# Optimization experiments

Measured on AMD Instinct MI355X. Metric: run time of the kernel, lower is better.

The kernel has to match this reference:

```python
import math
import jax, jax.numpy as jnp
import numpy as np

B, R, L_, K_, U_ = 64, 32, 64, 16, 4
DIMS = [2 * K_ * U_, 256, 256, K_]  # [input_dim] + hidden_dim + [output_dim]
BN_EPS = 1e-5


def _uniform_param(key, out_dim, in_dim):
    ini = math.sqrt(3.0 / out_dim / in_dim)
    return jax.random.uniform(key, (out_dim, in_dim), jnp.float32, -ini, ini)


def setup_inputs() -> dict:
    key = jax.random.key(0)
    ks = jax.random.split(key, 16)
    inp = {
        "Hhat_real": jax.random.normal(ks[0], (B, R, L_, K_, U_), jnp.float32),
        "Hhat_imag": jax.random.normal(ks[1], (B, R, L_, K_, U_), jnp.float32),
        "Vhat": jax.random.normal(ks[2], (B, R, L_, K_, U_), jnp.float32),
    }
    kidx = 3
    for i in range(len(DIMS) - 1):
        inp[f"P1_{i}"] = _uniform_param(ks[kidx], DIMS[i + 1], DIMS[i]); kidx += 1
        inp[f"P2_{i}"] = _uniform_param(ks[kidx], DIMS[i + 1], DIMS[i]); kidx += 1
        if i != len(DIMS) - 2:  # BN only on non-final layers
            inp[f"bn_w{i}"] = jnp.ones((DIMS[i + 1],), jnp.float32)
            inp[f"bn_b{i}"] = jnp.zeros((DIMS[i + 1],), jnp.float32)
    inp["nbrOfRealizations"] = R
    inp["L"] = L_
    inp["K"] = K_
    inp["U"] = U_
    return inp


def _layer(A, P1, P2, bn_w, bn_b, relu):
    # A: [N, C_in, L]
    A1 = jnp.einsum('oc,ncl->nol', P1, A)                       # [N, C_out, L]
    A2 = jnp.einsum('oc,nc->no', P2, A.mean(-1))[:, :, None]    # [N, C_out, 1]
    A = A1 + 0.1 * A2
    if relu:
        A = jax.nn.relu(A)
    if bn_w is not None:
        # BatchNorm1d (training mode): normalize over (N, L) per channel
        mu = A.mean(axis=(0, 2), keepdims=True)
        var = A.var(axis=(0, 2), keepdims=True)
        A = (A - mu) * jax.lax.rsqrt(var + BN_EPS) * bn_w[None, :, None] + bn_b[None, :, None]
    return A


def reference(Hhat_real, Hhat_imag, Vhat,
              P1_0, P2_0, bn_w0, bn_b0,
              P1_1, P2_1, bn_w1, bn_b1,
              P1_2, P2_2,
              nbrOfRealizations, L, K, U):
    Bsz = Hhat_real.shape[0]
    N = Bsz * nbrOfRealizations

    def prep(X):
        # view(N,1,L,K,U).transpose(2,3).transpose(3,4) -> [N,1,K,U,L]
        return jnp.transpose(X.reshape(N, 1, L, K, U), (0, 1, 3, 4, 2))

    A = jnp.concatenate([prep(Hhat_real), prep(Hhat_imag)], axis=1).reshape(N, 2 * K * U, L)
    A = _layer(A, P1_0, P2_0, bn_w0, bn_b0, relu=True)
    A = _layer(A, P1_1, P2_1, bn_w1, bn_b1, relu=True)
    A = _layer(A, P1_2, P2_2, None, None, relu=False)

    Phat_u1 = jnp.transpose(A.reshape(Bsz, nbrOfRealizations, K, L), (0, 1, 3, 2))  # [B,R,L,K]
    nrm = jnp.linalg.norm(Phat_u1, axis=2, keepdims=True)                            # [B,R,1,K]
    Phat_u = Phat_u1 / nrm * jnp.float32(math.sqrt(L))
    Fhat_u = Vhat.reshape(Bsz, nbrOfRealizations, L, K, U) * Phat_u[..., None]
    return Fhat_u
```

## Files before the change

kernel.cpp:

```cpp
#include <hip/hip_runtime.h>

typedef unsigned short ushort_t;
typedef unsigned int uint_t;

typedef short bf16x8 __attribute__((ext_vector_type(8)));
typedef float f32x4 __attribute__((ext_vector_type(4)));
#define MFMA16(a, b, c) __builtin_amdgcn_mfma_f32_16x16x32_bf16(a, b, c, 0, 0, 0)

__device__ __forceinline__ float bf2f(uint_t u) { return __uint_as_float(u << 16); }
__device__ __forceinline__ ushort_t f2bf(float f) {
  uint_t x = __float_as_uint(f);
  return (ushort_t)((x + 0x7fffu + ((x >> 16) & 1u)) >> 16);
}
__device__ __forceinline__ uint_t cvtpk(float lo, float hi) {
  uint_t r;
  asm("v_cvt_pk_bf16_f32 %0, %1, %2" : "=v"(r) : "v"(lo), "v"(hi));
  return r;
}
__device__ __forceinline__ void gload_lds16(const void* g, void* l) {
  __builtin_amdgcn_global_load_lds(
      (const __attribute__((address_space(1))) unsigned int*)g,
      (__attribute__((address_space(3))) unsigned int*)l, 16, 0, 0);
}

#define NBATCH 2048

__global__ __launch_bounds__(256) void pre0_kernel(
    const float* __restrict__ Hr, const float* __restrict__ Hi,
    const float* __restrict__ P2_0, const float* __restrict__ P1_0,
    ushort_t* __restrict__ W0bf, float* __restrict__ V20)
{
  __shared__ float r[4][128];
  __shared__ float hm[128];
  const int t = threadIdx.x, n = blockIdx.x;
  if (n < 128) {
    int i = n * 256 + t;
    W0bf[i] = f2bf(P1_0[i]);
  }
  const int q = t >> 6;
  const int c = (2 * t) & 127;
  const int cc = c & 63;
  const float* src = ((c < 64) ? Hr : Hi) + (size_t)n * 4096 + cc;
  float s0 = 0.f, s1 = 0.f;
  #pragma unroll
  for (int i = 0; i < 16; i++) {
    int l = 4 * i + q;
    float2 x = *(const float2*)(src + l * 64);
    s0 += x.x; s1 += x.y;
  }
  r[q][c] = s0; r[q][c + 1] = s1;
  __syncthreads();
  if (t < 128) hm[t] = (r[0][t] + r[1][t] + r[2][t] + r[3][t]) * (1.0f / 64.0f);
  __syncthreads();
  const float4* pw = (const float4*)(P2_0 + t * 128);
  float s = 0.f;
  #pragma unroll 8
  for (int c4 = 0; c4 < 32; c4++) {
    float4 p = pw[c4];
    s = fmaf(p.x, hm[4 * c4 + 0], s);
    s = fmaf(p.y, hm[4 * c4 + 1], s);
    s = fmaf(p.z, hm[4 * c4 + 2], s);
    s = fmaf(p.w, hm[4 * c4 + 3], s);
  }
  V20[n * 256 + t] = 0.1f * s;
}

__global__ __launch_bounds__(256) void layer0_mfma_kernel(
    const float* __restrict__ Hr, const float* __restrict__ Hi,
    const ushort_t* __restrict__ W0bf, const float* __restrict__ V20,
    ushort_t* __restrict__ Z, float* __restrict__ partA, float* __restrict__ partB)
{
  __shared__ __align__(16) ushort_t lds[64 * 264];
  float* ldsf = (float*)lds;
  const int t = threadIdx.x, n = blockIdx.x;
  const int lane = t & 63, w = t >> 6, r16 = lane & 15, g4 = lane >> 4;

  #pragma unroll
  for (int i = 0; i < 8; i++) {
    int G = (w * 8 + i) * 64 + lane;
    int row = G >> 5;
    int gc = G & 31;
    int gsrc = gc ^ (row & 7);
    int fi = gsrc * 4;
    const float* src = ((fi < 64) ? Hr : Hi) + (size_t)n * 4096 + row * 64 + (fi & 63);
    gload_lds16(src, &ldsf[(w * 8 + i) * 256]);
  }

  float4 v2r[4];
  #pragma unroll
  for (int m = 0; m < 4; m++)
    v2r[m] = *(const float4*)(V20 + n * 256 + w * 64 + m * 16 + g4 * 4);

  f32x4 acc[4][4];
  #pragma unroll
  for (int i = 0; i < 4; i++)
    #pragma unroll
    for (int j = 0; j < 4; j++) acc[i][j] = (f32x4){0.f, 0.f, 0.f, 0.f};

  __syncthreads();

  const int sw = r16 & 7;
  #pragma unroll
  for (int kk = 0; kk < 4; kk++) {
    bf16x8 aF[4], bF[4];
    #pragma unroll
    for (int m = 0; m < 4; m++)
      aF[m] = *(const bf16x8*)(W0bf + (w * 64 + m * 16 + r16) * 128 + kk * 32 + g4 * 8);
    #pragma unroll
    for (int nt = 0; nt < 4; nt++) {
      const int row = nt * 16 + r16;
      const float* base = ldsf + row * 128;
      const int g0 = kk * 8 + g4 * 2;
      float4 xa = *(const float4*)(base + ((g0 ^ sw) * 4));
      float4 xb = *(const float4*)(base + (((g0 + 1) ^ sw) * 4));
      uint4 u = make_uint4(cvtpk(xa.x, xa.y), cvtpk(xa.z, xa.w),
                           cvtpk(xb.x, xb.y), cvtpk(xb.z, xb.w));
      bF[nt] = *(const bf16x8*)&u;
    }
    #pragma unroll
    for (int m = 0; m < 4; m++)
      #pragma unroll
      for (int nt = 0; nt < 4; nt++)
        acc[m][nt] = MFMA16(aF[m], bF[nt], acc[m][nt]);
  }

  #pragma unroll
  for (int m = 0; m < 4; m++) {
    float s[4] = {0.f, 0.f, 0.f, 0.f}, q[4] = {0.f, 0.f, 0.f, 0.f};
    #pragma unroll
    for (int nt = 0; nt < 4; nt++)
      #pragma unroll
      for (int r = 0; r < 4; r++) {
        float v = fmaxf(acc[m][nt][r] + v2r[m][r], 0.f);
        s[r] += v; q[r] = fmaf(v, v, q[r]);
      }
    #pragma unroll
    for (int b = 1; b < 16; b <<= 1)
      #pragma unroll
      for (int r = 0; r < 4; r++) {
        s[r] += __shfl_xor(s[r], b);
        q[r] += __shfl_xor(q[r], b);
      }
    const int ob = w * 64 + m * 16 + g4 * 4;
    #pragma unroll
    for (int r = 0; r < 4; r++)
      if (r16 == r) {
        partA[n * 256 + ob + r] = s[r];
        partB[n * 256 + ob + r] = q[r];
      }
  }

  __syncthreads();
  #pragma unroll
  for (int m = 0; m < 4; m++) {
    const int ob = w * 64 + m * 16 + g4 * 4;
    #pragma unroll
    for (int nt = 0; nt < 4; nt++) {
      const int l = nt * 16 + r16;
      uint_t p0 = cvtpk(fmaxf(acc[m][nt][0] + v2r[m].x, 0.f),
                        fmaxf(acc[m][nt][1] + v2r[m].y, 0.f));
      uint_t p1 = cvtpk(fmaxf(acc[m][nt][2] + v2r[m].z, 0.f),
                        fmaxf(acc[m][nt][3] + v2r[m].w, 0.f));
      *(uint2*)(&lds[l * 264 + ob]) = make_uint2(p0, p1);
    }
  }
  __syncthreads();
  #pragma unroll
  for (int i = 0; i < 8; i++) {
    int el = i * 2048 + t * 8;
    int l = el >> 8, o0 = el & 255;
    *(uint4*)(&Z[(size_t)n * 16384 + el]) = *(const uint4*)(&lds[l * 264 + o0]);
  }
}

__global__ __launch_bounds__(256) void statsfin_kernel(
    const float* __restrict__ partA, const float* __restrict__ partB,
    const float* __restrict__ bnw, const float* __restrict__ bnb,
    float* __restrict__ stats)
{
  __shared__ float s1s[256], s2s[256];
  const int c = blockIdx.x, t = threadIdx.x;
  float s1 = 0.f, s2 = 0.f;
  #pragma unroll
  for (int j = 0; j < 8; j++) {
    int n = t * 8 + j;
    s1 += partA[n * 256 + c];
    s2 += partB[n * 256 + c];
  }
  s1s[t] = s1; s2s[t] = s2;
  __syncthreads();
  for (int s = 128; s > 0; s >>= 1) {
    if (t < s) { s1s[t] += s1s[t + s]; s2s[t] += s2s[t + s]; }
    __syncthreads();
  }
  if (t == 0) {
    const float inv = 1.0f / 131072.0f;
    float mu = s1s[0] * inv;
    float var = fmaxf(s2s[0] * inv - mu * mu, 0.f);
    float rstd = rsqrtf(var + 1e-5f);
    float sc = rstd * bnw[c];
    stats[2 * c]     = sc;
    stats[2 * c + 1] = bnb[c] - mu * sc;
  }
}

__global__ __launch_bounds__(256) void prep_kernel(
    const float* __restrict__ P1f, const float* __restrict__ P2f,
    const float* __restrict__ stats, ushort_t* __restrict__ Wbf,
    float* __restrict__ P2s, float* __restrict__ biasT)
{
  const int o = blockIdx.x, t = threadIdx.x;
  float sc = stats[2 * t], sh = stats[2 * t + 1];
  float w = P1f[o * 256 + t];
  Wbf[o * 256 + t] = f2bf(w * sc);
  float p = P2f[o * 256 + t];
  P2s[o * 256 + t] = p * sc;
  __shared__ float s1[256], s2[256];
  s1[t] = w * sh;
  s2[t] = p * sh;
  __syncthreads();
  for (int s = 128; s > 0; s >>= 1) {
    if (t < s) { s1[t] += s1[t + s]; s2[t] += s2[t + s]; }
    __syncthreads();
  }
  if (t == 0) biasT[o] = s1[0] + 0.1f * s2[0];
}

__global__ __launch_bounds__(256) void v2n_kernel(
    const float* __restrict__ partA, const float* __restrict__ P2s,
    const float* __restrict__ biasT, float* __restrict__ V2)
{
  __shared__ float zm[4][256];
  const int t = threadIdx.x, n0 = blockIdx.x * 4;
  #pragma unroll
  for (int j = 0; j < 4; j++) zm[j][t] = partA[(n0 + j) * 256 + t] * (1.0f / 64.0f);
  __syncthreads();
  float s[4] = {0.f, 0.f, 0.f, 0.f};
  const float4* pw = (const float4*)(P2s + t * 256);
  #pragma unroll 4
  for (int c4 = 0; c4 < 64; c4++) {
    float4 p = pw[c4];
    #pragma unroll
    for (int j = 0; j < 4; j++) {
      s[j] = fmaf(p.x, zm[j][4 * c4 + 0], s[j]);
      s[j] = fmaf(p.y, zm[j][4 * c4 + 1], s[j]);
      s[j] = fmaf(p.z, zm[j][4 * c4 + 2], s[j]);
      s[j] = fmaf(p.w, zm[j][4 * c4 + 3], s[j]);
    }
  }
  float b = biasT[t];
  #pragma unroll
  for (int j = 0; j < 4; j++) V2[(n0 + j) * 256 + t] = 0.1f * s[j] + b;
}

__global__ __launch_bounds__(256) void layer1_mfma_kernel(
    ushort_t* Z, const ushort_t* __restrict__ W1bf, const float* __restrict__ V21,
    float* __restrict__ partA, float* __restrict__ partB)
{
  __shared__ __align__(16) ushort_t lds[64 * 264];
  const int t = threadIdx.x, n = blockIdx.x;
  const int lane = t & 63, w = t >> 6, r16 = lane & 15, g4 = lane >> 4;
  const size_t zbase = (size_t)n * 16384;

  #pragma unroll
  for (int i = 0; i < 8; i++) {
    int G = (w * 8 + i) * 64 + lane;
    int row = G >> 5;
    int gc = G & 31;
    int gsrc = gc ^ (row & 7);
    gload_lds16(Z + zbase + row * 256 + gsrc * 8, &lds[(w * 8 + i) * 512]);
  }

  float4 v2r[4];
  #pragma unroll
  for (int m = 0; m < 4; m++)
    v2r[m] = *(const float4*)(V21 + n * 256 + w * 64 + m * 16 + g4 * 4);

  f32x4 acc[4][4];
  #pragma unroll
  for (int i = 0; i < 4; i++)
    #pragma unroll
    for (int j = 0; j < 4; j++) acc[i][j] = (f32x4){0.f, 0.f, 0.f, 0.f};

  bf16x8 aF[2][4];
  #pragma unroll
  for (int m = 0; m < 4; m++)
    aF[0][m] = *(const bf16x8*)(W1bf + (w * 64 + m * 16 + r16) * 256 + g4 * 8);

  __syncthreads();

  const int sw = r16 & 7;
  #pragma unroll
  for (int kk = 0; kk < 8; kk++) {
    const int cur = kk & 1, nxt = cur ^ 1;
    if (kk < 7) {
      #pragma unroll
      for (int m = 0; m < 4; m++)
        aF[nxt][m] = *(const bf16x8*)(W1bf + (w * 64 + m * 16 + r16) * 256 + (kk + 1) * 32 + g4 * 8);
    }
    bf16x8 bF[4];
    #pragma unroll
    for (int nt = 0; nt < 4; nt++) {
      const int row = nt * 16 + r16;
      bF[nt] = *(const bf16x8*)(&lds[row * 256 + (((kk * 4 + g4) ^ sw) * 8)]);
    }
    #pragma unroll
    for (int m = 0; m < 4; m++)
      #pragma unroll
      for (int nt = 0; nt < 4; nt++)
        acc[m][nt] = MFMA16(aF[cur][m], bF[nt], acc[m][nt]);
  }

  #pragma unroll
  for (int m = 0; m < 4; m++) {
    float s[4] = {0.f, 0.f, 0.f, 0.f}, q[4] = {0.f, 0.f, 0.f, 0.f};
    #pragma unroll
    for (int nt = 0; nt < 4; nt++)
      #pragma unroll
      for (int r = 0; r < 4; r++) {
        float v = fmaxf(acc[m][nt][r] + v2r[m][r], 0.f);
        s[r] += v; q[r] = fmaf(v, v, q[r]);
      }
    #pragma unroll
    for (int b = 1; b < 16; b <<= 1)
      #pragma unroll
      for (int r = 0; r < 4; r++) {
        s[r] += __shfl_xor(s[r], b);
        q[r] += __shfl_xor(q[r], b);
      }
    const int ob = w * 64 + m * 16 + g4 * 4;
    #pragma unroll
    for (int r = 0; r < 4; r++)
      if (r16 == r) {
        partA[n * 256 + ob + r] = s[r];
        partB[n * 256 + ob + r] = q[r];
      }
  }

  __syncthreads();
  #pragma unroll
  for (int m = 0; m < 4; m++) {
    const int ob = w * 64 + m * 16 + g4 * 4;
    #pragma unroll
    for (int nt = 0; nt < 4; nt++) {
      const int l = nt * 16 + r16;
      uint_t p0 = cvtpk(fmaxf(acc[m][nt][0] + v2r[m].x, 0.f),
                        fmaxf(acc[m][nt][1] + v2r[m].y, 0.f));
      uint_t p1 = cvtpk(fmaxf(acc[m][nt][2] + v2r[m].z, 0.f),
                        fmaxf(acc[m][nt][3] + v2r[m].w, 0.f));
      *(uint2*)(&lds[l * 264 + ob]) = make_uint2(p0, p1);
    }
  }
  __syncthreads();
  #pragma unroll
  for (int i = 0; i < 8; i++) {
    int el = i * 2048 + t * 8;
    int l = el >> 8, o0 = el & 255;
    *(uint4*)(&Z[zbase + el]) = *(const uint4*)(&lds[l * 264 + o0]);
  }
}

__global__ __launch_bounds__(256) void layer2final_kernel(
    const ushort_t* __restrict__ Z, const ushort_t* __restrict__ W2bf,
    const float* __restrict__ partA, const float* __restrict__ P2s2,
    const float* __restrict__ biasT2, const float* __restrict__ Vh,
    float* __restrict__ out)
{
  __shared__ float zm[256];
  __shared__ float red[16][17];
  __shared__ float v2s[16];
  __shared__ float zf[16][65];
  __shared__ float invn[16];
  const int t = threadIdx.x, n = blockIdx.x;
  const int lane = t & 63, w = t >> 6, r16 = lane & 15, g4 = lane >> 4;
  const size_t zbase = (size_t)n * 16384;

  zm[t] = partA[n * 256 + t] * (1.0f / 64.0f);

  f32x4 acc = (f32x4){0.f, 0.f, 0.f, 0.f};
  #pragma unroll 2
  for (int kk = 0; kk < 8; kk++) {
    bf16x8 aF = *(const bf16x8*)(W2bf + r16 * 256 + kk * 32 + g4 * 8);
    bf16x8 bF = *(const bf16x8*)(Z + zbase + (w * 16 + r16) * 256 + kk * 32 + g4 * 8);
    acc = MFMA16(aF, bF, acc);
  }
  __syncthreads();
  {
    const int oi = t & 15, ch = t >> 4;
    const float4* pw = (const float4*)(P2s2 + oi * 256 + ch * 16);
    float s = 0.f;
    #pragma unroll
    for (int c4 = 0; c4 < 4; c4++) {
      float4 p = pw[c4];
      int cb = ch * 16 + c4 * 4;
      s = fmaf(p.x, zm[cb + 0], s);
      s = fmaf(p.y, zm[cb + 1], s);
      s = fmaf(p.z, zm[cb + 2], s);
      s = fmaf(p.w, zm[cb + 3], s);
    }
    red[ch][oi] = s;
  }
  __syncthreads();
  if (t < 16) {
    float a = 0.f;
    #pragma unroll
    for (int c = 0; c < 16; c++) a += red[c][t];
    v2s[t] = 0.1f * a + biasT2[t];
  }
  __syncthreads();
  #pragma unroll
  for (int r = 0; r < 4; r++) {
    int o = g4 * 4 + r;
    zf[o][w * 16 + r16] = acc[r] + v2s[o];
  }
  __syncthreads();
  if (t < 16) {
    float s = 0.f;
    #pragma unroll
    for (int l = 0; l < 64; l++) s = fmaf(zf[t][l], zf[t][l], s);
    invn[t] = (s > 0.f) ? (8.0f * rsqrtf(s)) : 0.f;
  }
  __syncthreads();
  const size_t base = (size_t)n * 4096;
  #pragma unroll
  for (int g = 0; g < 4; g++) {
    int e = t * 16 + g * 4;
    int l = e >> 6;
    int k = (e >> 2) & 15;
    float val = zf[k][l] * invn[k];
    float4 vv = *(const float4*)(Vh + base + e);
    *(float4*)(out + base + e) =
        make_float4(vv.x * val, vv.y * val, vv.z * val, vv.w * val);
  }
}

extern "C" void kernel_launch(void* const* d_in, const int* in_sizes, int n_in,
                              void* d_out, int out_size, void* d_ws, size_t ws_size,
                              hipStream_t stream) {
  const float* Hr   = (const float*)d_in[0];
  const float* Hi   = (const float*)d_in[1];
  const float* Vh   = (const float*)d_in[2];
  const float* P1_0 = (const float*)d_in[3];
  const float* P2_0 = (const float*)d_in[4];
  const float* bnw0 = (const float*)d_in[5];
  const float* bnb0 = (const float*)d_in[6];
  const float* P1_1 = (const float*)d_in[7];
  const float* P2_1 = (const float*)d_in[8];
  const float* bnw1 = (const float*)d_in[9];
  const float* bnb1 = (const float*)d_in[10];
  const float* P1_2 = (const float*)d_in[11];
  const float* P2_2 = (const float*)d_in[12];

  char* ws = (char*)d_ws;
  float*    stats0 = (float*)   (ws);
  float*    stats1 = (float*)   (ws + 2048);
  float*    biasT  = (float*)   (ws + 4096);
  float*    biasT2 = (float*)   (ws + 5120);
  ushort_t* W0bf   = (ushort_t*)(ws + 8192);
  ushort_t* W1bf   = (ushort_t*)(ws + 73728);
  ushort_t* W2bf   = (ushort_t*)(ws + 204800);
  float*    P2s1   = (float*)   (ws + 212992);
  float*    P2s2   = (float*)   (ws + 475136);
  float*    partA  = (float*)   (ws + 491520);
  float*    partB  = (float*)   (ws + 2588672);
  float*    V20    = (float*)   (ws + 4685824);
  float*    V21    = (float*)   (ws + 6782976);
  ushort_t* Z      = (ushort_t*)(ws + 9437184);

  pre0_kernel<<<NBATCH, 256, 0, stream>>>(Hr, Hi, P2_0, P1_0, W0bf, V20);
  layer0_mfma_kernel<<<NBATCH, 256, 0, stream>>>(Hr, Hi, W0bf, V20, Z, partA, partB);
  statsfin_kernel<<<256, 256, 0, stream>>>(partA, partB, bnw0, bnb0, stats0);
  prep_kernel<<<256, 256, 0, stream>>>(P1_1, P2_1, stats0, W1bf, P2s1, biasT);
  v2n_kernel<<<512, 256, 0, stream>>>(partA, P2s1, biasT, V21);
  layer1_mfma_kernel<<<NBATCH, 256, 0, stream>>>(Z, W1bf, V21, partA, partB);
  statsfin_kernel<<<256, 256, 0, stream>>>(partA, partB, bnw1, bnb1, stats1);
  prep_kernel<<<16, 256, 0, stream>>>(P1_2, P2_2, stats1, W2bf, P2s2, biasT2);
  layer2final_kernel<<<NBATCH, 256, 0, stream>>>(Z, W2bf, partA, P2s2, biasT2, Vh, (float*)d_out);
}
```

Baseline: 206.7 us.

## Process two samples per block with double-buffered LDS prefetch in layers 0 and 1

Layer 0 and layer 1 MFMA kernels now handle two consecutive samples per block. Both samples get their own LDS buffer, and the second sample's global-to-LDS load is issued while the first sample is computed and written out. The grid is halved to match. The aim is to hide global load latency inside the block, at the cost of doubling LDS per block, which lowers the number of resident blocks per CU and halves the block count.

```diff
diff --git a/kernel.cpp b/kernel.cpp
--- a/kernel.cpp
+++ b/kernel.cpp
@@ -70,106 +70,116 @@
     const ushort_t* __restrict__ W0bf, const float* __restrict__ V20,
     ushort_t* __restrict__ Z, float* __restrict__ partA, float* __restrict__ partB)
 {
-  __shared__ __align__(16) ushort_t lds[64 * 264];
-  float* ldsf = (float*)lds;
-  const int t = threadIdx.x, n = blockIdx.x;
+  __shared__ __align__(16) ushort_t lds[2][64 * 264];
+  const int t = threadIdx.x, nb = blockIdx.x;
   const int lane = t & 63, w = t >> 6, r16 = lane & 15, g4 = lane >> 4;
-
-  #pragma unroll
-  for (int i = 0; i < 8; i++) {
-    int G = (w * 8 + i) * 64 + lane;
-    int row = G >> 5;
-    int gc = G & 31;
-    int gsrc = gc ^ (row & 7);
-    int fi = gsrc * 4;
-    const float* src = ((fi < 64) ? Hr : Hi) + (size_t)n * 4096 + row * 64 + (fi & 63);
-    gload_lds16(src, &ldsf[(w * 8 + i) * 256]);
-  }
-
-  float4 v2r[4];
-  #pragma unroll
-  for (int m = 0; m < 4; m++)
-    v2r[m] = *(const float4*)(V20 + n * 256 + w * 64 + m * 16 + g4 * 4);
-
-  f32x4 acc[4][4];
-  #pragma unroll
-  for (int i = 0; i < 4; i++)
-    #pragma unroll
-    for (int j = 0; j < 4; j++) acc[i][j] = (f32x4){0.f, 0.f, 0.f, 0.f};
-
-  __syncthreads();
-
   const int sw = r16 & 7;
-  #pragma unroll
-  for (int kk = 0; kk < 4; kk++) {
-    bf16x8 aF[4], bF[4];
+
+  auto stageH = [&](float* bufF, int n) {
+    #pragma unroll
+    for (int i = 0; i < 8; i++) {
+      int G = (w * 8 + i) * 64 + lane;
+      int row = G >> 5;
+      int gc = G & 31;
+      int gsrc = gc ^ (row & 7);
+      int fi = gsrc * 4;
+      const float* src = ((fi < 64) ? Hr : Hi) + (size_t)n * 4096 + row * 64 + (fi & 63);
+      gload_lds16(src, bufF + (w * 8 + i) * 256);
+    }
+  };
+
+  stageH((float*)&lds[0][0], 2 * nb);
+  __syncthreads();
+  stageH((float*)&lds[1][0], 2 * nb + 1);
+
+  #pragma unroll
+  for (int half = 0; half < 2; half++) {
+    const int n = 2 * nb + half;
+    ushort_t* buf = &lds[half][0];
+    float* bufF = (float*)buf;
+
+    float4 v2r[4];
     #pragma unroll
     for (int m = 0; m < 4; m++)
-      aF[m] = *(const bf16x8*)(W0bf + (w * 64 + m * 16 + r16) * 128 + kk * 32 + g4 * 8);
-    #pragma unroll
-    for (int nt = 0; nt < 4; nt++) {
-      const int row = nt * 16 + r16;
-      const float* base = ldsf + row * 128;
-      const int g0 = kk * 8 + g4 * 2;
-      float4 xa = *(const float4*)(base + ((g0 ^ sw) * 4));
-      float4 xb = *(const float4*)(base + (((g0 + 1) ^ sw) * 4));
-      uint4 u = make_uint4(cvtpk(xa.x, xa.y), cvtpk(xa.z, xa.w),
-                           cvtpk(xb.x, xb.y), cvtpk(xb.z, xb.w));
-      bF[nt] = *(const bf16x8*)&u;
-    }
-    #pragma unroll
-    for (int m = 0; m < 4; m++)
+      v2r[m] = *(const float4*)(V20 + n * 256 + w * 64 + m * 16 + g4 * 4);
+
+    f32x4 acc[4][4];
+    #pragma unroll
+    for (int i = 0; i < 4; i++)
+      #pragma unroll
+      for (int j = 0; j < 4; j++) acc[i][j] = (f32x4){0.f, 0.f, 0.f, 0.f};
+
+    #pragma unroll
+    for (int kk = 0; kk < 4; kk++) {
+      bf16x8 aF[4], bF[4];
+      #pragma unroll
+      for (int m = 0; m < 4; m++)
+        aF[m] = *(const bf16x8*)(W0bf + (w * 64 + m * 16 + r16) * 128 + kk * 32 + g4 * 8);
+      #pragma unroll
+      for (int nt = 0; nt < 4; nt++) {
+        const int row = nt * 16 + r16;
+        const float* base = bufF + row * 128;
+        const int g0 = kk * 8 + g4 * 2;
+        float4 xa = *(const float4*)(base + ((g0 ^ sw) * 4));
+        float4 xb = *(const float4*)(base + (((g0 + 1) ^ sw) * 4));
+        uint4 u = make_uint4(cvtpk(xa.x, xa.y), cvtpk(xa.z, xa.w),
+                             cvtpk(xb.x, xb.y), cvtpk(xb.z, xb.w));
+        bF[nt] = *(const bf16x8*)&u;
+      }
+      #pragma unroll
+      for (int m = 0; m < 4; m++)
+        #pragma unroll
+        for (int nt = 0; nt < 4; nt++)
+          acc[m][nt] = MFMA16(aF[m], bF[nt], acc[m][nt]);
+    }
+
+    #pragma unroll
+    for (int m = 0; m < 4; m++) {
+      float s[4] = {0.f, 0.f, 0.f, 0.f}, q[4] = {0.f, 0.f, 0.f, 0.f};
       #pragma unroll
       for (int nt = 0; nt < 4; nt++)
-        acc[m][nt] = MFMA16(aF[m], bF[nt], acc[m][nt]);
-  }
-
-  #pragma unroll
-  for (int m = 0; m < 4; m++) {
-    float s[4] = {0.f, 0.f, 0.f, 0.f}, q[4] = {0.f, 0.f, 0.f, 0.f};
-    #pragma unroll
-    for (int nt = 0; nt < 4; nt++)
-      #pragma unroll
-      for (int r = 0; r < 4; r++) {
-        float v = fmaxf(acc[m][nt][r] + v2r[m][r], 0.f);
-        s[r] += v; q[r] = fmaf(v, v, q[r]);
+        #pragma unroll
+        for (int r = 0; r < 4; r++) {
+          float v = fmaxf(acc[m][nt][r] + v2r[m][r], 0.f);
+          s[r] += v; q[r] = fmaf(v, v, q[r]);
+        }
+      #pragma unroll
+      for (int b = 1; b < 16; b <<= 1)
+        #pragma unroll
+        for (int r = 0; r < 4; r++) {
+          s[r] += __shfl_xor(s[r], b);
+          q[r] += __shfl_xor(q[r], b);
+        }
+      const int ob = w * 64 + m * 16 + g4 * 4;
+      #pragma unroll
+      for (int r = 0; r < 4; r++)
+        if (r16 == r) {
+          partA[n * 256 + ob + r] = s[r];
+          partB[n * 256 + ob + r] = q[r];
+        }
+    }
+
+    __syncthreads();
+    #pragma unroll
+    for (int m = 0; m < 4; m++) {
+      const int ob = w * 64 + m * 16 + g4 * 4;
+      #pragma unroll
+      for (int nt = 0; nt < 4; nt++) {
+        const int l = nt * 16 + r16;
+        uint_t p0 = cvtpk(fmaxf(acc[m][nt][0] + v2r[m].x, 0.f),
+                          fmaxf(acc[m][nt][1] + v2r[m].y, 0.f));
+        uint_t p1 = cvtpk(fmaxf(acc[m][nt][2] + v2r[m].z, 0.f),
+                          fmaxf(acc[m][nt][3] + v2r[m].w, 0.f));
+        *(uint2*)(&buf[l * 264 + ob]) = make_uint2(p0, p1);
       }
-    #pragma unroll
-    for (int b = 1; b < 16; b <<= 1)
-      #pragma unroll
-      for (int r = 0; r < 4; r++) {
-        s[r] += __shfl_xor(s[r], b);
-        q[r] += __shfl_xor(q[r], b);
-      }
-    const int ob = w * 64 + m * 16 + g4 * 4;
-    #pragma unroll
-    for (int r = 0; r < 4; r++)
-      if (r16 == r) {
-        partA[n * 256 + ob + r] = s[r];
-        partB[n * 256 + ob + r] = q[r];
-      }
-  }
-
-  __syncthreads();
-  #pragma unroll
-  for (int m = 0; m < 4; m++) {
-    const int ob = w * 64 + m * 16 + g4 * 4;
-    #pragma unroll
-    for (int nt = 0; nt < 4; nt++) {
-      const int l = nt * 16 + r16;
-      uint_t p0 = cvtpk(fmaxf(acc[m][nt][0] + v2r[m].x, 0.f),
-                        fmaxf(acc[m][nt][1] + v2r[m].y, 0.f));
-      uint_t p1 = cvtpk(fmaxf(acc[m][nt][2] + v2r[m].z, 0.f),
-                        fmaxf(acc[m][nt][3] + v2r[m].w, 0.f));
-      *(uint2*)(&lds[l * 264 + ob]) = make_uint2(p0, p1);
-    }
-  }
-  __syncthreads();
-  #pragma unroll
-  for (int i = 0; i < 8; i++) {
-    int el = i * 2048 + t * 8;
-    int l = el >> 8, o0 = el & 255;
-    *(uint4*)(&Z[(size_t)n * 16384 + el]) = *(const uint4*)(&lds[l * 264 + o0]);
+    }
+    __syncthreads();
+    #pragma unroll
+    for (int i = 0; i < 8; i++) {
+      int el = i * 2048 + t * 8;
+      int l = el >> 8, o0 = el & 255;
+      *(uint4*)(&Z[(size_t)n * 16384 + el]) = *(const uint4*)(&buf[l * 264 + o0]);
+    }
   }
 }
 
@@ -257,106 +267,117 @@
     ushort_t* Z, const ushort_t* __restrict__ W1bf, const float* __restrict__ V21,
     float* __restrict__ partA, float* __restrict__ partB)
 {
-  __shared__ __align__(16) ushort_t lds[64 * 264];
-  const int t = threadIdx.x, n = blockIdx.x;
+  __shared__ __align__(16) ushort_t lds[2][64 * 264];
+  const int t = threadIdx.x, nb = blockIdx.x;
   const int lane = t & 63, w = t >> 6, r16 = lane & 15, g4 = lane >> 4;
-  const size_t zbase = (size_t)n * 16384;
-
-  #pragma unroll
-  for (int i = 0; i < 8; i++) {
-    int G = (w * 8 + i) * 64 + lane;
-    int row = G >> 5;
-    int gc = G & 31;
-    int gsrc = gc ^ (row & 7);
-    gload_lds16(Z + zbase + row * 256 + gsrc * 8, &lds[(w * 8 + i) * 512]);
-  }
-
-  float4 v2r[4];
-  #pragma unroll
-  for (int m = 0; m < 4; m++)
-    v2r[m] = *(const float4*)(V21 + n * 256 + w * 64 + m * 16 + g4 * 4);
-
-  f32x4 acc[4][4];
-  #pragma unroll
-  for (int i = 0; i < 4; i++)
-    #pragma unroll
-    for (int j = 0; j < 4; j++) acc[i][j] = (f32x4){0.f, 0.f, 0.f, 0.f};
-
-  bf16x8 aF[2][4];
-  #pragma unroll
-  for (int m = 0; m < 4; m++)
-    aF[0][m] = *(const bf16x8*)(W1bf + (w * 64 + m * 16 + r16) * 256 + g4 * 8);
-
-  __syncthreads();
-
   const int sw = r16 & 7;
-  #pragma unroll
-  for (int kk = 0; kk < 8; kk++) {
-    const int cur = kk & 1, nxt = cur ^ 1;
-    if (kk < 7) {
+
+  auto stageZ = [&](ushort_t* buf, int n) {
+    const size_t zb = (size_t)n * 16384;
+    #pragma unroll
+    for (int i = 0; i < 8; i++) {
+      int G = (w * 8 + i) * 64 + lane;
+      int row = G >> 5;
+      int gc = G & 31;
+      int gsrc = gc ^ (row & 7);
+      gload_lds16(Z + zb + row * 256 + gsrc * 8, buf + (w * 8 + i) * 512);
+    }
+  };
+
+  stageZ(&lds[0][0], 2 * nb);
+  __syncthreads();
+  stageZ(&lds[1][0], 2 * nb + 1);
+
+  #pragma unroll
+  for (int half = 0; half < 2; half++) {
+    const int n = 2 * nb + half;
+    ushort_t* buf = &lds[half][0];
+    const size_t zbase = (size_t)n * 16384;
+
+    float4 v2r[4];
+    #pragma unroll
+    for (int m = 0; m < 4; m++)
+      v2r[m] = *(const float4*)(V21 + n * 256 + w * 64 + m * 16 + g4 * 4);
+
+    f32x4 acc[4][4];
+    #pragma unroll
+    for (int i = 0; i < 4; i++)
+      #pragma unroll
+      for (int j = 0; j < 4; j++) acc[i][j] = (f32x4){0.f, 0.f, 0.f, 0.f};
+
+    bf16x8 aF[2][4];
+    #pragma unroll
+    for (int m = 0; m < 4; m++)
+      aF[0][m] = *(const bf16x8*)(W1bf + (w * 64 + m * 16 + r16) * 256 + g4 * 8);
+
+    #pragma unroll
+    for (int kk = 0; kk < 8; kk++) {
+      const int cur = kk & 1, nxt = cur ^ 1;
+      if (kk < 7) {
+        #pragma unroll
+        for (int m = 0; m < 4; m++)
+          aF[nxt][m] = *(const bf16x8*)(W1bf + (w * 64 + m * 16 + r16) * 256 + (kk + 1) * 32 + g4 * 8);
+      }
+      bf16x8 bF[4];
+      #pragma unroll
+      for (int nt = 0; nt < 4; nt++) {
+        const int row = nt * 16 + r16;
+        bF[nt] = *(const bf16x8*)(&buf[row * 256 + (((kk * 4 + g4) ^ sw) * 8)]);
+      }
       #pragma unroll
       for (int m = 0; m < 4; m++)
-        aF[nxt][m] = *(const bf16x8*)(W1bf + (w * 64 + m * 16 + r16) * 256 + (kk + 1) * 32 + g4 * 8);
-    }
-    bf16x8 bF[4];
-    #pragma unroll
-    for (int nt = 0; nt < 4; nt++) {
-      const int row = nt * 16 + r16;
-      bF[nt] = *(const bf16x8*)(&lds[row * 256 + (((kk * 4 + g4) ^ sw) * 8)]);
-    }
-    #pragma unroll
-    for (int m = 0; m < 4; m++)
+        #pragma unroll
+        for (int nt = 0; nt < 4; nt++)
+          acc[m][nt] = MFMA16(aF[cur][m], bF[nt], acc[m][nt]);
+    }
+
+    #pragma unroll
+    for (int m = 0; m < 4; m++) {
+      float s[4] = {0.f, 0.f, 0.f, 0.f}, q[4] = {0.f, 0.f, 0.f, 0.f};
       #pragma unroll
       for (int nt = 0; nt < 4; nt++)
-        acc[m][nt] = MFMA16(aF[cur][m], bF[nt], acc[m][nt]);
-  }
-
-  #pragma unroll
-  for (int m = 0; m < 4; m++) {
-    float s[4] = {0.f, 0.f, 0.f, 0.f}, q[4] = {0.f, 0.f, 0.f, 0.f};
-    #pragma unroll
-    for (int nt = 0; nt < 4; nt++)
-      #pragma unroll
-      for (int r = 0; r < 4; r++) {
-        float v = fmaxf(acc[m][nt][r] + v2r[m][r], 0.f);
-        s[r] += v; q[r] = fmaf(v, v, q[r]);
+        #pragma unroll
+        for (int r = 0; r < 4; r++) {
+          float v = fmaxf(acc[m][nt][r] + v2r[m][r], 0.f);
+          s[r] += v; q[r] = fmaf(v, v, q[r]);
+        }
+      #pragma unroll
+      for (int b = 1; b < 16; b <<= 1)
+        #pragma unroll
+        for (int r = 0; r < 4; r++) {
+          s[r] += __shfl_xor(s[r], b);
+          q[r] += __shfl_xor(q[r], b);
+        }
+      const int ob = w * 64 + m * 16 + g4 * 4;
+      #pragma unroll
+      for (int r = 0; r < 4; r++)
+        if (r16 == r) {
+          partA[n * 256 + ob + r] = s[r];
+          partB[n * 256 + ob + r] = q[r];
+        }
+    }
+
+    __syncthreads();
+    #pragma unroll
+    for (int m = 0; m < 4; m++) {
+      const int ob = w * 64 + m * 16 + g4 * 4;
+      #pragma unroll
+      for (int nt = 0; nt < 4; nt++) {
+        const int l = nt * 16 + r16;
+        uint_t p0 = cvtpk(fmaxf(acc[m][nt][0] + v2r[m].x, 0.f),
+                          fmaxf(acc[m][nt][1] + v2r[m].y, 0.f));
+        uint_t p1 = cvtpk(fmaxf(acc[m][nt][2] + v2r[m].z, 0.f),
+                          fmaxf(acc[m][nt][3] + v2r[m].w, 0.f));
+        *(uint2*)(&buf[l * 264 + ob]) = make_uint2(p0, p1);
       }
-    #pragma unroll
-    for (int b = 1; b < 16; b <<= 1)
-      #pragma unroll
-      for (int r = 0; r < 4; r++) {
-        s[r] += __shfl_xor(s[r], b);
-        q[r] += __shfl_xor(q[r], b);
-      }
-    const int ob = w * 64 + m * 16 + g4 * 4;
-    #pragma unroll
-    for (int r = 0; r < 4; r++)
-      if (r16 == r) {
-        partA[n * 256 + ob + r] = s[r];
-        partB[n * 256 + ob + r] = q[r];
-      }
-  }
-
-  __syncthreads();
-  #pragma unroll
-  for (int m = 0; m < 4; m++) {
-    const int ob = w * 64 + m * 16 + g4 * 4;
-    #pragma unroll
-    for (int nt = 0; nt < 4; nt++) {
-      const int l = nt * 16 + r16;
-      uint_t p0 = cvtpk(fmaxf(acc[m][nt][0] + v2r[m].x, 0.f),
-                        fmaxf(acc[m][nt][1] + v2r[m].y, 0.f));
-      uint_t p1 = cvtpk(fmaxf(acc[m][nt][2] + v2r[m].z, 0.f),
-                        fmaxf(acc[m][nt][3] + v2r[m].w, 0.f));
-      *(uint2*)(&lds[l * 264 + ob]) = make_uint2(p0, p1);
-    }
-  }
-  __syncthreads();
-  #pragma unroll
-  for (int i = 0; i < 8; i++) {
-    int el = i * 2048 + t * 8;
-    int l = el >> 8, o0 = el & 255;
-    *(uint4*)(&Z[zbase + el]) = *(const uint4*)(&lds[l * 264 + o0]);
+    }
+    __syncthreads();
+    #pragma unroll
+    for (int i = 0; i < 8; i++) {
+      int el = i * 2048 + t * 8;
+      int l = el >> 8, o0 = el & 255;
+      *(uint4*)(&Z[zbase + el]) = *(const uint4*)(&buf[l * 264 + o0]);
+    }
   }
 }
 
@@ -468,11 +489,11 @@
   ushort_t* Z      = (ushort_t*)(ws + 9437184);
 
   pre0_kernel<<<NBATCH, 256, 0, stream>>>(Hr, Hi, P2_0, P1_0, W0bf, V20);
-  layer0_mfma_kernel<<<NBATCH, 256, 0, stream>>>(Hr, Hi, W0bf, V20, Z, partA, partB);
+  layer0_mfma_kernel<<<NBATCH / 2, 256, 0, stream>>>(Hr, Hi, W0bf, V20, Z, partA, partB);
   statsfin_kernel<<<256, 256, 0, stream>>>(partA, partB, bnw0, bnb0, stats0);
   prep_kernel<<<256, 256, 0, stream>>>(P1_1, P2_1, stats0, W1bf, P2s1, biasT);
   v2n_kernel<<<512, 256, 0, stream>>>(partA, P2s1, biasT, V21);
-  layer1_mfma_kernel<<<NBATCH, 256, 0, stream>>>(Z, W1bf, V21, partA, partB);
+  layer1_mfma_kernel<<<NBATCH / 2, 256, 0, stream>>>(Z, W1bf, V21, partA, partB);
   statsfin_kernel<<<256, 256, 0, stream>>>(partA, partB, bnw1, bnb1, stats1);
   prep_kernel<<<16, 256, 0, stream>>>(P1_2, P2_2, stats1, W2bf, P2s2, biasT2);
   layer2final_kernel<<<NBATCH, 256, 0, stream>>>(Z, W2bf, partA, P2s2, biasT2, Vh, (float*)d_out);
```

Measured after the change: 202.7 us. About the same (-1.9%).
